# Performance work log

Hardware: AMD Instinct MI355X
Metric: run time of the kernel (lower is better)

## Reference

```python
import jax, jax.numpy as jnp
import numpy as np

NUM_USERS = 100000
NUM_BOOKS = 100000
N = NUM_USERS + NUM_BOOKS
E = 2000000
EMB = 16
HID = 32


def setup_inputs() -> dict:
    key = jax.random.key(0)
    ks = jax.random.split(key, 16)
    node_idx = jnp.arange(N, dtype=jnp.int64 if jax.config.jax_enable_x64 else jnp.int32)
    node_type = (node_idx >= NUM_USERS).astype(node_idx.dtype)
    x = jnp.stack([node_idx, node_type], axis=1)  # [N, 2]
    edge_index = jax.random.randint(ks[0], (2, E), 0, N)
    edge_weight = jnp.ones((E,), jnp.float32)
    inp = {
        "x": x,
        "edge_index": edge_index,
        "edge_weight": edge_weight,
        "user_emb": jax.random.normal(ks[1], (NUM_USERS, EMB), jnp.float32) * 0.1,
        "book_emb": jax.random.normal(ks[2], (NUM_BOOKS, EMB), jnp.float32) * 0.1,
    }
    dims = [(EMB, HID), (HID, HID), (HID, HID), (HID, HID), (HID, HID), (HID, EMB)]
    for i, (di, do) in enumerate(dims):
        inp[f"W{i}"] = jax.random.normal(ks[3 + i], (di, do), jnp.float32) / np.sqrt(di)
        inp[f"b{i}"] = jnp.zeros((do,), jnp.float32)
    return inp


def _gcn_norm(edge_index, edge_weight, n):
    # add self loops with weight 1 (PyG GCNConv default)
    loops = jnp.arange(n, dtype=edge_index.dtype)
    row = jnp.concatenate([edge_index[0], loops])
    col = jnp.concatenate([edge_index[1], loops])
    w = jnp.concatenate([edge_weight, jnp.ones((n,), edge_weight.dtype)])
    deg = jax.ops.segment_sum(w, col, num_segments=n)
    dinv = jnp.where(deg > 0, jax.lax.rsqrt(jnp.maximum(deg, 1e-12)), 0.0)
    norm = dinv[row] * w * dinv[col]
    return row, col, norm


def _gcn_layer(h, W, b, row, col, norm, n):
    h = h @ W                              # [N, dout] linear first (PyG order)
    msg = h[row] * norm[:, None]           # gather + scale  [E+N, dout]
    agg = jax.ops.segment_sum(msg, col, num_segments=n)  # scatter-add
    return agg + b


def reference(x, edge_index, edge_weight, user_emb, book_emb,
              W0, b0, W1, b1, W2, b2, W3, b3, W4, b4, W5, b5):
    node_indices = x[:, 0]
    node_types = x[:, 1]
    is_user = (node_types == 0)
    u = user_emb[jnp.clip(node_indices, 0, NUM_USERS - 1)]
    b = book_emb[jnp.clip(node_indices - NUM_USERS, 0, NUM_BOOKS - 1)]
    h = jnp.where(is_user[:, None], u, b)  # [N, EMB]

    n = x.shape[0]
    row, col, norm = _gcn_norm(edge_index, edge_weight, n)

    Ws = [W0, W1, W2, W3, W4, W5]
    bs = [b0, b1, b2, b3, b4, b5]
    for i in range(5):
        h = _gcn_layer(h, Ws[i], bs[i], row, col, norm, n)
        h = jax.nn.relu(h)
        # dropout is identity in eval mode (training=False)
    h = _gcn_layer(h, Ws[5], bs[5], row, col, norm, n)
    return h
```

## Files before the change

kernel.cpp:

```cpp
#include <hip/hip_runtime.h>


namespace {

constexpr int kUsers = 100000;
constexpr int kBooks = 100000;
constexpr int kN = kUsers + kBooks;
constexpr int kE = 2000000;
constexpr int BLK = 256;

constexpr int SUBB = 512;
constexpr int NSUB = (kN + SUBB - 1) / SUBB;
constexpr int CAP2 = 5888;
constexpr int TILE = 8192;
constexpr int NTILES = (kE + TILE - 1) / TILE;

__global__ void init_kernel(int* __restrict__ bcur) {
  int gid = blockIdx.x * blockDim.x + threadIdx.x;
  if (gid < NSUB) bcur[gid] = 0;
}

__global__ void embed_kernel(const int* __restrict__ x,
                             const float* __restrict__ uemb,
                             const float* __restrict__ bemb,
                             float* __restrict__ h) {
  int gid = blockIdx.x * blockDim.x + threadIdx.x;
  int node = gid >> 2;
  int q = gid & 3;
  if (node >= kN) return;
  int2 xv = ((const int2*)x)[node];
  float4 v;
  if (xv.y == 0) {
    int c = min(max(xv.x, 0), kUsers - 1);
    v = ((const float4*)(uemb + (size_t)c * 16))[q];
  } else {
    int c = min(max(xv.x - kUsers, 0), kBooks - 1);
    v = ((const float4*)(bemb + (size_t)c * 16))[q];
  }
  ((float4*)h)[node * 4 + q] = v;
}

__global__ void __launch_bounds__(BLK) bucketize_kernel(
    const int* __restrict__ ei, const float* __restrict__ ew,
    int* __restrict__ bcur, int4* __restrict__ recs) {
  __shared__ int hist[NSUB];
  __shared__ int gcur[NSUB];
  int base = blockIdx.x * TILE;
  int end = min(kE, base + TILE);
  for (int i = threadIdx.x; i < NSUB; i += BLK) hist[i] = 0;
  __syncthreads();
  const int4* col4 = (const int4*)(ei + kE);
  for (int i = base / 4 + threadIdx.x; i < end / 4; i += BLK) {
    int4 c = col4[i];
    atomicAdd(&hist[c.x >> 9], 1);
    atomicAdd(&hist[c.y >> 9], 1);
    atomicAdd(&hist[c.z >> 9], 1);
    atomicAdd(&hist[c.w >> 9], 1);
  }
  __syncthreads();
  for (int i = threadIdx.x; i < NSUB; i += BLK)
    gcur[i] = atomicAdd(&bcur[i], hist[i]);
  __syncthreads();
  for (int i = base + threadIdx.x; i < end; i += BLK) {
    int r = ei[i];
    int c = ei[kE + i];
    float w = ew[i];
    int b = c >> 9;
    int pos = atomicAdd(&gcur[b], 1);
    pos = min(pos, CAP2 - 1);
    recs[(size_t)b * CAP2 + pos] = make_int4(r, c, __float_as_int(w), 0);
  }
}

__global__ void __launch_bounds__(BLK) build_kernel(
    const int4* __restrict__ recs, const int* __restrict__ bcur,
    int2* __restrict__ csr, int2* __restrict__ row_span,
    float* __restrict__ dinv) {
  __shared__ int cnt[SUBB];
  __shared__ int off[SUBB];
  __shared__ int cur[SUBB];
  __shared__ int tsum[BLK];
  __shared__ int2 stage[CAP2];
  int b = blockIdx.x;
  int lo = b * SUBB;
  int nloc = min(SUBB, kN - lo);
  int n = min(bcur[b], CAP2);
  const int4* rp = recs + (size_t)b * CAP2;
  int t = threadIdx.x;
  for (int i = t; i < SUBB; i += BLK) cnt[i] = 0;
  __syncthreads();
  for (int i = t; i < n; i += BLK) atomicAdd(&cnt[rp[i].y - lo], 1);
  __syncthreads();
  int a0 = cnt[2 * t], a1 = cnt[2 * t + 1];
  tsum[t] = a0 + a1;
  __syncthreads();
  for (int o = 1; o < BLK; o <<= 1) {
    int v = (t >= o) ? tsum[t - o] : 0;
    __syncthreads();
    tsum[t] += v;
    __syncthreads();
  }
  int tb = (t == 0) ? 0 : tsum[t - 1];
  off[2 * t] = tb;
  off[2 * t + 1] = tb + a0;
  cur[2 * t] = tb;
  cur[2 * t + 1] = tb + a0;
  __syncthreads();
  int padbase = b * CAP2;
  for (int i = t; i < nloc; i += BLK)
    row_span[lo + i] = make_int2(padbase + off[i], padbase + off[i] + cnt[i]);
  for (int i = t; i < n; i += BLK) {
    int4 rec = rp[i];
    int p = atomicAdd(&cur[rec.y - lo], 1);
    stage[p] = make_int2(rec.x, rec.z);
  }
  __syncthreads();
  for (int i = t; i < nloc; i += BLK) {
    float s = 1.0f;
    int e1 = off[i] + cnt[i];
    for (int e = off[i]; e < e1; ++e) s += __int_as_float(stage[e].y);
    dinv[lo + i] = rsqrtf(fmaxf(s, 1e-12f));
  }
  for (int i = t; i < n; i += BLK) csr[padbase + i] = stage[i];
}

__global__ void __launch_bounds__(BLK) prenorm_kernel(
    int2* __restrict__ csr, const int* __restrict__ bcur,
    const float* __restrict__ dinv) {
  int b = blockIdx.x;
  int n = min(bcur[b], CAP2);
  int base = b * CAP2;
  for (int i = threadIdx.x; i < n; i += BLK) {
    int2 rec = csr[base + i];
    csr[base + i].y =
        __float_as_int(dinv[rec.x] * __int_as_float(rec.y));
  }
}

template <int LANES, int DOUT, bool RELU, bool CHAIN16>
__global__ void __launch_bounds__(BLK) layer_kernel(
    const float* __restrict__ h, float* __restrict__ outp,
    const int2* __restrict__ row_span, const int2* __restrict__ csr,
    const float* __restrict__ dinv, const float* __restrict__ W,
    const float* __restrict__ bias, const float* __restrict__ W2) {
  constexpr int DIN = LANES * 4;
  constexpr int OPL = DOUT / LANES;
  __shared__ float sW[DIN * DOUT];
  __shared__ float sB[DOUT];
  __shared__ float sW2[CHAIN16 ? 32 * 16 : 1];
  for (int i = threadIdx.x; i < DIN * DOUT; i += BLK) sW[i] = W[i];
  for (int i = threadIdx.x; i < DOUT; i += BLK) sB[i] = bias[i];
  if (CHAIN16)
    for (int i = threadIdx.x; i < 32 * 16; i += BLK) sW2[i] = W2[i];
  __syncthreads();

  int gid = blockIdx.x * BLK + threadIdx.x;
  int node = gid / LANES;
  int lane = gid % LANES;
  if (node >= kN) return;
  float di = dinv[node];
  const float4* h4 = (const float4*)h;
  float4 hs = h4[node * LANES + lane];
  int2 span = row_span[node];
  float4 a0 = make_float4(0.f, 0.f, 0.f, 0.f), a1 = a0, a2 = a0, a3 = a0;
  int e = span.x;
  for (; e + 3 < span.y; e += 4) {
    int2 r0 = csr[e], r1 = csr[e + 1], r2 = csr[e + 2], r3 = csr[e + 3];
    float4 h0 = h4[r0.x * LANES + lane];
    float4 h1 = h4[r1.x * LANES + lane];
    float4 h2 = h4[r2.x * LANES + lane];
    float4 h3 = h4[r3.x * LANES + lane];
    float w0 = __int_as_float(r0.y), w1 = __int_as_float(r1.y);
    float w2 = __int_as_float(r2.y), w3 = __int_as_float(r3.y);
    a0.x = fmaf(h0.x, w0, a0.x); a0.y = fmaf(h0.y, w0, a0.y);
    a0.z = fmaf(h0.z, w0, a0.z); a0.w = fmaf(h0.w, w0, a0.w);
    a1.x = fmaf(h1.x, w1, a1.x); a1.y = fmaf(h1.y, w1, a1.y);
    a1.z = fmaf(h1.z, w1, a1.z); a1.w = fmaf(h1.w, w1, a1.w);
    a2.x = fmaf(h2.x, w2, a2.x); a2.y = fmaf(h2.y, w2, a2.y);
    a2.z = fmaf(h2.z, w2, a2.z); a2.w = fmaf(h2.w, w2, a2.w);
    a3.x = fmaf(h3.x, w3, a3.x); a3.y = fmaf(h3.y, w3, a3.y);
    a3.z = fmaf(h3.z, w3, a3.z); a3.w = fmaf(h3.w, w3, a3.w);
  }
  for (; e < span.y; ++e) {
    int2 rc = csr[e];
    float w = __int_as_float(rc.y);
    float4 hv = h4[rc.x * LANES + lane];
    a0.x = fmaf(hv.x, w, a0.x); a0.y = fmaf(hv.y, w, a0.y);
    a0.z = fmaf(hv.z, w, a0.z); a0.w = fmaf(hv.w, w, a0.w);
  }
  float ax = ((a0.x + a1.x) + (a2.x + a3.x) + hs.x * di) * di;
  float ay = ((a0.y + a1.y) + (a2.y + a3.y) + hs.y * di) * di;
  float az = ((a0.z + a1.z) + (a2.z + a3.z) + hs.z * di) * di;
  float aw = ((a0.w + a1.w) + (a2.w + a3.w) + hs.w * di) * di;

  float o[OPL];
#pragma unroll
  for (int j = 0; j < OPL; ++j) o[j] = sB[lane * OPL + j];
#pragma unroll
  for (int k = 0; k < DIN; ++k) {
    const int c = k & 3;
    float v = (c == 0) ? ax : (c == 1) ? ay : (c == 2) ? az : aw;
    float hk = __shfl(v, k >> 2, LANES);
    const float* wr = &sW[k * DOUT + lane * OPL];
#pragma unroll
    for (int j = 0; j < OPL; ++j) o[j] = fmaf(hk, wr[j], o[j]);
  }
  if (RELU) {
#pragma unroll
    for (int j = 0; j < OPL; ++j) o[j] = fmaxf(o[j], 0.f);
  }
  if (!CHAIN16) {
    float* op = outp + (size_t)node * DOUT + lane * OPL;
#pragma unroll
    for (int j = 0; j < OPL; j += 4)
      *(float4*)(op + j) = make_float4(o[j], o[j + 1], o[j + 2], o[j + 3]);
  } else {
    float o2x = 0.f, o2y = 0.f;
#pragma unroll
    for (int k = 0; k < 32; ++k) {
      const int c = k & 3;
      float v = (c == 0) ? o[0] : (c == 1) ? o[1] : (c == 2) ? o[2] : o[3];
      float hk = __shfl(v, k >> 2, 8);
      o2x = fmaf(hk, sW2[k * 16 + lane * 2 + 0], o2x);
      o2y = fmaf(hk, sW2[k * 16 + lane * 2 + 1], o2y);
    }
    *(float2*)(outp + (size_t)node * 16 + lane * 2) = make_float2(o2x, o2y);
  }
}

__global__ void __launch_bounds__(BLK) final_prop_kernel(
    const float* __restrict__ h, float* __restrict__ out,
    const int2* __restrict__ row_span, const int2* __restrict__ csr,
    const float* __restrict__ dinv, const float* __restrict__ b5) {
  int gid = blockIdx.x * BLK + threadIdx.x;
  int node = gid >> 2;
  int q = gid & 3;
  if (node >= kN) return;
  float di = dinv[node];
  const float4* h4 = (const float4*)h;
  float4 hs = h4[node * 4 + q];
  int2 span = row_span[node];
  float4 a0 = make_float4(0.f, 0.f, 0.f, 0.f), a1 = a0, a2 = a0, a3 = a0;
  int e = span.x;
  for (; e + 3 < span.y; e += 4) {
    int2 r0 = csr[e], r1 = csr[e + 1], r2 = csr[e + 2], r3 = csr[e + 3];
    float4 h0 = h4[r0.x * 4 + q];
    float4 h1 = h4[r1.x * 4 + q];
    float4 h2 = h4[r2.x * 4 + q];
    float4 h3 = h4[r3.x * 4 + q];
    float w0 = __int_as_float(r0.y), w1 = __int_as_float(r1.y);
    float w2 = __int_as_float(r2.y), w3 = __int_as_float(r3.y);
    a0.x = fmaf(h0.x, w0, a0.x); a0.y = fmaf(h0.y, w0, a0.y);
    a0.z = fmaf(h0.z, w0, a0.z); a0.w = fmaf(h0.w, w0, a0.w);
    a1.x = fmaf(h1.x, w1, a1.x); a1.y = fmaf(h1.y, w1, a1.y);
    a1.z = fmaf(h1.z, w1, a1.z); a1.w = fmaf(h1.w, w1, a1.w);
    a2.x = fmaf(h2.x, w2, a2.x); a2.y = fmaf(h2.y, w2, a2.y);
    a2.z = fmaf(h2.z, w2, a2.z); a2.w = fmaf(h2.w, w2, a2.w);
    a3.x = fmaf(h3.x, w3, a3.x); a3.y = fmaf(h3.y, w3, a3.y);
    a3.z = fmaf(h3.z, w3, a3.z); a3.w = fmaf(h3.w, w3, a3.w);
  }
  for (; e < span.y; ++e) {
    int2 rc = csr[e];
    float w = __int_as_float(rc.y);
    float4 hv = h4[rc.x * 4 + q];
    a0.x = fmaf(hv.x, w, a0.x); a0.y = fmaf(hv.y, w, a0.y);
    a0.z = fmaf(hv.z, w, a0.z); a0.w = fmaf(hv.w, w, a0.w);
  }
  float4 b = ((const float4*)b5)[q];
  float4 r;
  r.x = ((a0.x + a1.x) + (a2.x + a3.x) + hs.x * di) * di + b.x;
  r.y = ((a0.y + a1.y) + (a2.y + a3.y) + hs.y * di) * di + b.y;
  r.z = ((a0.z + a1.z) + (a2.z + a3.z) + hs.z * di) * di + b.z;
  r.w = ((a0.w + a1.w) + (a2.w + a3.w) + hs.w * di) * di + b.w;
  ((float4*)out)[node * 4 + q] = r;
}

inline int cdiv(long a, long b) { return (int)((a + b - 1) / b); }

}

extern "C" void kernel_launch(void* const* d_in, const int* in_sizes, int n_in,
                              void* d_out, int out_size, void* d_ws,
                              size_t ws_size, hipStream_t stream) {
  const int* x = (const int*)d_in[0];
  const int* ei = (const int*)d_in[1];
  const float* ew = (const float*)d_in[2];
  const float* uemb = (const float*)d_in[3];
  const float* bemb = (const float*)d_in[4];
  const float* W0 = (const float*)d_in[5];
  const float* b0 = (const float*)d_in[6];
  const float* W1 = (const float*)d_in[7];
  const float* b1 = (const float*)d_in[8];
  const float* W2 = (const float*)d_in[9];
  const float* b2 = (const float*)d_in[10];
  const float* W3 = (const float*)d_in[11];
  const float* b3 = (const float*)d_in[12];
  const float* W4 = (const float*)d_in[13];
  const float* b4 = (const float*)d_in[14];
  const float* W5 = (const float*)d_in[15];
  const float* b5 = (const float*)d_in[16];
  float* out = (float*)d_out;

  char* ws = (char*)d_ws;
  size_t off = 0;
  auto walloc = [&](size_t bytes) -> void* {
    void* p = ws + off;
    off += (bytes + 255) & ~size_t(255);
    return p;
  };
  int2* row_span = (int2*)walloc((size_t)kN * 8);
  float* dinv = (float*)walloc((size_t)kN * 4);
  int* bcur = (int*)walloc((size_t)NSUB * 4);
  int2* csr = (int2*)walloc((size_t)NSUB * CAP2 * 8);
  float* hA = (float*)walloc((size_t)kN * 32 * 4);
  float* hB = (float*)walloc((size_t)kN * 32 * 4);
  int4* recs = (int4*)hA;
  float* hE = hA;
  float* hE2 = hB;
  (void)ws_size;
  (void)in_sizes;
  (void)n_in;
  (void)out_size;

  init_kernel<<<cdiv(NSUB, BLK), BLK, 0, stream>>>(bcur);
  bucketize_kernel<<<NTILES, BLK, 0, stream>>>(ei, ew, bcur, recs);
  build_kernel<<<NSUB, BLK, 0, stream>>>(recs, bcur, csr, row_span, dinv);
  prenorm_kernel<<<NSUB, BLK, 0, stream>>>(csr, bcur, dinv);
  embed_kernel<<<kN * 4 / BLK, BLK, 0, stream>>>(x, uemb, bemb, hE);

  layer_kernel<4, 32, true, false><<<kN * 4 / BLK, BLK, 0, stream>>>(
      hE, hB, row_span, csr, dinv, W0, b0, nullptr);
  layer_kernel<8, 32, true, false><<<kN * 8 / BLK, BLK, 0, stream>>>(
      hB, hA, row_span, csr, dinv, W1, b1, nullptr);
  layer_kernel<8, 32, true, false><<<kN * 8 / BLK, BLK, 0, stream>>>(
      hA, hB, row_span, csr, dinv, W2, b2, nullptr);
  layer_kernel<8, 32, true, false><<<kN * 8 / BLK, BLK, 0, stream>>>(
      hB, hA, row_span, csr, dinv, W3, b3, nullptr);
  layer_kernel<8, 32, true, true><<<kN * 8 / BLK, BLK, 0, stream>>>(
      hA, hE2, row_span, csr, dinv, W4, b4, W5);
  final_prop_kernel<<<kN * 4 / BLK, BLK, 0, stream>>>(hE2, out, row_span, csr,
                                                      dinv, b5);
}
```

Before: 465.7 us.

## Sort nodes by degree within each bucket and unroll gather loop to 8

```diff
diff --git a/kernel.cpp b/kernel.cpp
--- a/kernel.cpp
+++ b/kernel.cpp
@@ -75,11 +75,12 @@
 __global__ void __launch_bounds__(BLK) build_kernel(
     const int4* __restrict__ recs, const int* __restrict__ bcur,
     int2* __restrict__ csr, int2* __restrict__ row_span,
-    float* __restrict__ dinv) {
+    float* __restrict__ dinv, int* __restrict__ nodeperm) {
   __shared__ int cnt[SUBB];
   __shared__ int off[SUBB];
   __shared__ int cur[SUBB];
   __shared__ int tsum[BLK];
+  __shared__ int hist2[64];
   __shared__ int2 stage[CAP2];
   int b = blockIdx.x;
   int lo = b * SUBB;
@@ -88,6 +89,7 @@
   const int4* rp = recs + (size_t)b * CAP2;
   int t = threadIdx.x;
   for (int i = t; i < SUBB; i += BLK) cnt[i] = 0;
+  if (t < 64) hist2[t] = 0;
   __syncthreads();
   for (int i = t; i < n; i += BLK) atomicAdd(&cnt[rp[i].y - lo], 1);
   __syncthreads();
@@ -114,7 +116,21 @@
     int p = atomicAdd(&cur[rec.y - lo], 1);
     stage[p] = make_int2(rec.x, rec.z);
   }
-  __syncthreads();
+  for (int i = t; i < nloc; i += BLK) atomicAdd(&hist2[min(cnt[i], 63)], 1);
+  __syncthreads();
+  if (t == 0) {
+    int run = 0;
+    for (int j = 0; j < 64; ++j) {
+      int v = hist2[j];
+      hist2[j] = run;
+      run += v;
+    }
+  }
+  __syncthreads();
+  for (int i = t; i < nloc; i += BLK) {
+    int r = atomicAdd(&hist2[min(cnt[i], 63)], 1);
+    nodeperm[lo + r] = lo + i;
+  }
   for (int i = t; i < nloc; i += BLK) {
     float s = 1.0f;
     int e1 = off[i] + cnt[i];
@@ -132,17 +148,23 @@
   int base = b * CAP2;
   for (int i = threadIdx.x; i < n; i += BLK) {
     int2 rec = csr[base + i];
-    csr[base + i].y =
-        __float_as_int(dinv[rec.x] * __int_as_float(rec.y));
-  }
-}
+    csr[base + i].y = __float_as_int(dinv[rec.x] * __int_as_float(rec.y));
+  }
+}
+
+#define FMA4(A, H, W_)                \
+  A.x = fmaf(H.x, W_, A.x);           \
+  A.y = fmaf(H.y, W_, A.y);           \
+  A.z = fmaf(H.z, W_, A.z);           \
+  A.w = fmaf(H.w, W_, A.w);
 
 template <int LANES, int DOUT, bool RELU, bool CHAIN16>
 __global__ void __launch_bounds__(BLK) layer_kernel(
     const float* __restrict__ h, float* __restrict__ outp,
     const int2* __restrict__ row_span, const int2* __restrict__ csr,
-    const float* __restrict__ dinv, const float* __restrict__ W,
-    const float* __restrict__ bias, const float* __restrict__ W2) {
+    const float* __restrict__ dinv, const int* __restrict__ nodeperm,
+    const float* __restrict__ W, const float* __restrict__ bias,
+    const float* __restrict__ W2) {
   constexpr int DIN = LANES * 4;
   constexpr int OPL = DOUT / LANES;
   __shared__ float sW[DIN * DOUT];
@@ -155,43 +177,46 @@
   __syncthreads();
 
   int gid = blockIdx.x * BLK + threadIdx.x;
-  int node = gid / LANES;
+  int grp = gid / LANES;
   int lane = gid % LANES;
-  if (node >= kN) return;
+  if (grp >= kN) return;
+  int node = nodeperm[grp];
   float di = dinv[node];
   const float4* h4 = (const float4*)h;
   float4 hs = h4[node * LANES + lane];
   int2 span = row_span[node];
-  float4 a0 = make_float4(0.f, 0.f, 0.f, 0.f), a1 = a0, a2 = a0, a3 = a0;
+  float4 A0 = make_float4(0.f, 0.f, 0.f, 0.f), A1 = A0, A2 = A0, A3 = A0;
   int e = span.x;
-  for (; e + 3 < span.y; e += 4) {
+  for (; e + 7 < span.y; e += 8) {
     int2 r0 = csr[e], r1 = csr[e + 1], r2 = csr[e + 2], r3 = csr[e + 3];
+    int2 r4 = csr[e + 4], r5 = csr[e + 5], r6 = csr[e + 6], r7 = csr[e + 7];
     float4 h0 = h4[r0.x * LANES + lane];
     float4 h1 = h4[r1.x * LANES + lane];
     float4 h2 = h4[r2.x * LANES + lane];
     float4 h3 = h4[r3.x * LANES + lane];
-    float w0 = __int_as_float(r0.y), w1 = __int_as_float(r1.y);
-    float w2 = __int_as_float(r2.y), w3 = __int_as_float(r3.y);
-    a0.x = fmaf(h0.x, w0, a0.x); a0.y = fmaf(h0.y, w0, a0.y);
-    a0.z = fmaf(h0.z, w0, a0.z); a0.w = fmaf(h0.w, w0, a0.w);
-    a1.x = fmaf(h1.x, w1, a1.x); a1.y = fmaf(h1.y, w1, a1.y);
-    a1.z = fmaf(h1.z, w1, a1.z); a1.w = fmaf(h1.w, w1, a1.w);
-    a2.x = fmaf(h2.x, w2, a2.x); a2.y = fmaf(h2.y, w2, a2.y);
-    a2.z = fmaf(h2.z, w2, a2.z); a2.w = fmaf(h2.w, w2, a2.w);
-    a3.x = fmaf(h3.x, w3, a3.x); a3.y = fmaf(h3.y, w3, a3.y);
-    a3.z = fmaf(h3.z, w3, a3.z); a3.w = fmaf(h3.w, w3, a3.w);
+    float4 h4v = h4[r4.x * LANES + lane];
+    float4 h5 = h4[r5.x * LANES + lane];
+    float4 h6 = h4[r6.x * LANES + lane];
+    float4 h7 = h4[r7.x * LANES + lane];
+    FMA4(A0, h0, __int_as_float(r0.y));
+    FMA4(A1, h1, __int_as_float(r1.y));
+    FMA4(A2, h2, __int_as_float(r2.y));
+    FMA4(A3, h3, __int_as_float(r3.y));
+    FMA4(A0, h4v, __int_as_float(r4.y));
+    FMA4(A1, h5, __int_as_float(r5.y));
+    FMA4(A2, h6, __int_as_float(r6.y));
+    FMA4(A3, h7, __int_as_float(r7.y));
   }
   for (; e < span.y; ++e) {
     int2 rc = csr[e];
     float w = __int_as_float(rc.y);
     float4 hv = h4[rc.x * LANES + lane];
-    a0.x = fmaf(hv.x, w, a0.x); a0.y = fmaf(hv.y, w, a0.y);
-    a0.z = fmaf(hv.z, w, a0.z); a0.w = fmaf(hv.w, w, a0.w);
-  }
-  float ax = ((a0.x + a1.x) + (a2.x + a3.x) + hs.x * di) * di;
-  float ay = ((a0.y + a1.y) + (a2.y + a3.y) + hs.y * di) * di;
-  float az = ((a0.z + a1.z) + (a2.z + a3.z) + hs.z * di) * di;
-  float aw = ((a0.w + a1.w) + (a2.w + a3.w) + hs.w * di) * di;
+    FMA4(A0, hv, w);
+  }
+  float ax = ((A0.x + A1.x) + (A2.x + A3.x) + hs.x * di) * di;
+  float ay = ((A0.y + A1.y) + (A2.y + A3.y) + hs.y * di) * di;
+  float az = ((A0.z + A1.z) + (A2.z + A3.z) + hs.z * di) * di;
+  float aw = ((A0.w + A1.w) + (A2.w + A3.w) + hs.w * di) * di;
 
   float o[OPL];
 #pragma unroll
@@ -231,47 +256,51 @@
 __global__ void __launch_bounds__(BLK) final_prop_kernel(
     const float* __restrict__ h, float* __restrict__ out,
     const int2* __restrict__ row_span, const int2* __restrict__ csr,
-    const float* __restrict__ dinv, const float* __restrict__ b5) {
+    const float* __restrict__ dinv, const int* __restrict__ nodeperm,
+    const float* __restrict__ b5) {
   int gid = blockIdx.x * BLK + threadIdx.x;
-  int node = gid >> 2;
+  int grp = gid >> 2;
   int q = gid & 3;
-  if (node >= kN) return;
+  if (grp >= kN) return;
+  int node = nodeperm[grp];
   float di = dinv[node];
   const float4* h4 = (const float4*)h;
   float4 hs = h4[node * 4 + q];
   int2 span = row_span[node];
-  float4 a0 = make_float4(0.f, 0.f, 0.f, 0.f), a1 = a0, a2 = a0, a3 = a0;
+  float4 A0 = make_float4(0.f, 0.f, 0.f, 0.f), A1 = A0, A2 = A0, A3 = A0;
   int e = span.x;
-  for (; e + 3 < span.y; e += 4) {
+  for (; e + 7 < span.y; e += 8) {
     int2 r0 = csr[e], r1 = csr[e + 1], r2 = csr[e + 2], r3 = csr[e + 3];
+    int2 r4 = csr[e + 4], r5 = csr[e + 5], r6 = csr[e + 6], r7 = csr[e + 7];
     float4 h0 = h4[r0.x * 4 + q];
     float4 h1 = h4[r1.x * 4 + q];
     float4 h2 = h4[r2.x * 4 + q];
     float4 h3 = h4[r3.x * 4 + q];
-    float w0 = __int_as_float(r0.y), w1 = __int_as_float(r1.y);
-    float w2 = __int_as_float(r2.y), w3 = __int_as_float(r3.y);
-    a0.x = fmaf(h0.x, w0, a0.x); a0.y = fmaf(h0.y, w0, a0.y);
-    a0.z = fmaf(h0.z, w0, a0.z); a0.w = fmaf(h0.w, w0, a0.w);
-    a1.x = fmaf(h1.x, w1, a1.x); a1.y = fmaf(h1.y, w1, a1.y);
-    a1.z = fmaf(h1.z, w1, a1.z); a1.w = fmaf(h1.w, w1, a1.w);
-    a2.x = fmaf(h2.x, w2, a2.x); a2.y = fmaf(h2.y, w2, a2.y);
-    a2.z = fmaf(h2.z, w2, a2.z); a2.w = fmaf(h2.w, w2, a2.w);
-    a3.x = fmaf(h3.x, w3, a3.x); a3.y = fmaf(h3.y, w3, a3.y);
-    a3.z = fmaf(h3.z, w3, a3.z); a3.w = fmaf(h3.w, w3, a3.w);
+    float4 h4v = h4[r4.x * 4 + q];
+    float4 h5 = h4[r5.x * 4 + q];
+    float4 h6 = h4[r6.x * 4 + q];
+    float4 h7 = h4[r7.x * 4 + q];
+    FMA4(A0, h0, __int_as_float(r0.y));
+    FMA4(A1, h1, __int_as_float(r1.y));
+    FMA4(A2, h2, __int_as_float(r2.y));
+    FMA4(A3, h3, __int_as_float(r3.y));
+    FMA4(A0, h4v, __int_as_float(r4.y));
+    FMA4(A1, h5, __int_as_float(r5.y));
+    FMA4(A2, h6, __int_as_float(r6.y));
+    FMA4(A3, h7, __int_as_float(r7.y));
   }
   for (; e < span.y; ++e) {
     int2 rc = csr[e];
     float w = __int_as_float(rc.y);
     float4 hv = h4[rc.x * 4 + q];
-    a0.x = fmaf(hv.x, w, a0.x); a0.y = fmaf(hv.y, w, a0.y);
-    a0.z = fmaf(hv.z, w, a0.z); a0.w = fmaf(hv.w, w, a0.w);
+    FMA4(A0, hv, w);
   }
   float4 b = ((const float4*)b5)[q];
   float4 r;
-  r.x = ((a0.x + a1.x) + (a2.x + a3.x) + hs.x * di) * di + b.x;
-  r.y = ((a0.y + a1.y) + (a2.y + a3.y) + hs.y * di) * di + b.y;
-  r.z = ((a0.z + a1.z) + (a2.z + a3.z) + hs.z * di) * di + b.z;
-  r.w = ((a0.w + a1.w) + (a2.w + a3.w) + hs.w * di) * di + b.w;
+  r.x = ((A0.x + A1.x) + (A2.x + A3.x) + hs.x * di) * di + b.x;
+  r.y = ((A0.y + A1.y) + (A2.y + A3.y) + hs.y * di) * di + b.y;
+  r.z = ((A0.z + A1.z) + (A2.z + A3.z) + hs.z * di) * di + b.z;
+  r.w = ((A0.w + A1.w) + (A2.w + A3.w) + hs.w * di) * di + b.w;
   ((float4*)out)[node * 4 + q] = r;
 }
 
@@ -310,6 +339,7 @@
   };
   int2* row_span = (int2*)walloc((size_t)kN * 8);
   float* dinv = (float*)walloc((size_t)kN * 4);
+  int* nodeperm = (int*)walloc((size_t)kN * 4);
   int* bcur = (int*)walloc((size_t)NSUB * 4);
   int2* csr = (int2*)walloc((size_t)NSUB * CAP2 * 8);
   float* hA = (float*)walloc((size_t)kN * 32 * 4);
@@ -324,20 +354,21 @@
 
   init_kernel<<<cdiv(NSUB, BLK), BLK, 0, stream>>>(bcur);
   bucketize_kernel<<<NTILES, BLK, 0, stream>>>(ei, ew, bcur, recs);
-  build_kernel<<<NSUB, BLK, 0, stream>>>(recs, bcur, csr, row_span, dinv);
+  build_kernel<<<NSUB, BLK, 0, stream>>>(recs, bcur, csr, row_span, dinv,
+                                         nodeperm);
   prenorm_kernel<<<NSUB, BLK, 0, stream>>>(csr, bcur, dinv);
   embed_kernel<<<kN * 4 / BLK, BLK, 0, stream>>>(x, uemb, bemb, hE);
 
   layer_kernel<4, 32, true, false><<<kN * 4 / BLK, BLK, 0, stream>>>(
-      hE, hB, row_span, csr, dinv, W0, b0, nullptr);
+      hE, hB, row_span, csr, dinv, nodeperm, W0, b0, nullptr);
   layer_kernel<8, 32, true, false><<<kN * 8 / BLK, BLK, 0, stream>>>(
-      hB, hA, row_span, csr, dinv, W1, b1, nullptr);
+      hB, hA, row_span, csr, dinv, nodeperm, W1, b1, nullptr);
   layer_kernel<8, 32, true, false><<<kN * 8 / BLK, BLK, 0, stream>>>(
-      hA, hB, row_span, csr, dinv, W2, b2, nullptr);
+      hA, hB, row_span, csr, dinv, nodeperm, W2, b2, nullptr);
   layer_kernel<8, 32, true, false><<<kN * 8 / BLK, BLK, 0, stream>>>(
-      hB, hA, row_span, csr, dinv, W3, b3, nullptr);
+      hB, hA, row_span, csr, dinv, nodeperm, W3, b3, nullptr);
   layer_kernel<8, 32, true, true><<<kN * 8 / BLK, BLK, 0, stream>>>(
-      hA, hE2, row_span, csr, dinv, W4, b4, W5);
+      hA, hE2, row_span, csr, dinv, nodeperm, W4, b4, W5);
   final_prop_kernel<<<kN * 4 / BLK, BLK, 0, stream>>>(hE2, out, row_span, csr,
-                                                      dinv, b5);
-}
+                                                      dinv, nodeperm, b5);
+}
```

Result: slower. 554.3 us (+19.0%).
